# Performance work log

Measured on AMD Instinct MI355X. Metric: run time of the kernel, lower is better.

Reference implementation:

```python
import jax, jax.numpy as jnp
import numpy as np

Q_HEADS, KV_HEADS, DIMS = 16, 4, 1024
HEAD_DIM = DIMS // Q_HEADS          # 64
GROUPS = Q_HEADS // KV_HEADS        # 4
ROPE_BASE = 10000.0


def rope(x):
    # x: (..., s, d) -- standard interleaved rotary embedding, base 10000
    s, d = x.shape[-2], x.shape[-1]
    inv_freq = 1.0 / (ROPE_BASE ** (jnp.arange(0, d, 2, dtype=jnp.float32) / d))
    ang = jnp.arange(s, dtype=jnp.float32)[:, None] * inv_freq[None, :]  # (s, d/2)
    cos, sin = jnp.cos(ang), jnp.sin(ang)
    x1, x2 = x[..., 0::2], x[..., 1::2]
    out = jnp.stack([x1 * cos - x2 * sin, x1 * sin + x2 * cos], axis=-1)
    return out.reshape(x.shape).astype(x.dtype)


def setup_inputs() -> dict:
    key = jax.random.key(0)
    k1, k2, k3, k4, k5, k6 = jax.random.split(key, 6)
    B, S, E = 4, 2048, 1024
    q = jax.random.normal(k1, (B, S, E), dtype=jnp.float32)
    kv = jax.random.normal(k2, (B, S, E), dtype=jnp.float32)
    sc = 1.0 / np.sqrt(E)
    Wq = jax.random.normal(k3, (E, Q_HEADS, HEAD_DIM), dtype=jnp.float32) * sc
    Wk = jax.random.normal(k4, (E, KV_HEADS, HEAD_DIM), dtype=jnp.float32) * sc
    Wv = jax.random.normal(k5, (E, KV_HEADS, HEAD_DIM), dtype=jnp.float32) * sc
    Wo = jax.random.normal(k6, (HEAD_DIM, E), dtype=jnp.float32) / np.sqrt(HEAD_DIM)
    return {"q": q, "kv": kv, "Wq": Wq, "Wk": Wk, "Wv": Wv, "Wo": Wo}


def reference(q, kv, Wq, Wk, Wv, Wo):
    B, S, E = q.shape
    qh = jnp.einsum('bse,ehd->bshd', q, Wq)    # (B,S,Q_HEADS,hd)
    kh = jnp.einsum('bse,ehd->bshd', kv, Wk)   # (B,S,KV_HEADS,hd)
    vh = jnp.einsum('bse,ehd->bshd', kv, Wv)
    # rearrange '... s (h g) d -> ... g h s d' with g=GROUPS (h = KV_HEADS outer)
    qh = qh.reshape(B, S, KV_HEADS, GROUPS, HEAD_DIM).transpose(0, 3, 2, 1, 4)  # (B,g,h,S,d)
    kh = kh.transpose(0, 2, 1, 3)  # (B,h,S,d)
    vh = vh.transpose(0, 2, 1, 3)  # (B,h,S,d)
    qh = rope(qh)
    kh = rope(kh)
    # NOTE: sums over group axis g (faithful to original einsum)
    scores = jnp.einsum('bghsd,bhad->bhsa', qh, kh)
    attn = jax.nn.softmax(scores / (HEAD_DIM ** 0.5), axis=-1)
    out = jnp.einsum('bhsa,bhad->bhsd', attn, vh)  # (B,h,S,d)
    out = out.mean(axis=1)                          # mean over kv heads -> (B,S,d)
    return out @ Wo                                 # (B,S,E)
```

## Files before the change

### kernel.cpp

```cpp
#include <hip/hip_runtime.h>
#include <math.h>

#define SS 2048
#define EE 1024

using bf16x8 = __attribute__((ext_vector_type(8))) short;
using f32x4  = __attribute__((ext_vector_type(4))) float;

__device__ inline short f2bf(float x) {
    unsigned u = __builtin_bit_cast(unsigned, x);
    return (short)((u + 0x7fffu + ((u >> 16) & 1u)) >> 16);
}
__device__ inline short f2bf_r(float x) {
    return (short)((__builtin_bit_cast(unsigned, x) + 0x8000u) >> 16);
}
__device__ inline unsigned pk_bf16(float a, float b) {
    unsigned ua = __builtin_bit_cast(unsigned, a) + 0x8000u;
    unsigned ub = __builtin_bit_cast(unsigned, b) + 0x8000u;
    return __builtin_amdgcn_perm(ub, ua, 0x07060302u);
}
__device__ inline void gl16(const short* g, short* l) {
    __builtin_amdgcn_global_load_lds(
        (const __attribute__((address_space(1))) void*)g,
        (__attribute__((address_space(3))) void*)l, 16, 0, 0);
}

__global__ __launch_bounds__(256) void prep_weights(const float* __restrict__ q,
                                                    const float* __restrict__ kv,
                                                    const float* __restrict__ Wq,
                                                    const float* __restrict__ Wk,
                                                    const float* __restrict__ Wv,
                                                    const float* __restrict__ Wo,
                                                    short* __restrict__ Ab,
                                                    short* __restrict__ Wall,
                                                    short* __restrict__ Wo4,
                                                    float2* __restrict__ RT) {
    if (blockIdx.x < 8192) {
        int gt = blockIdx.x * 256 + threadIdx.x;
        size_t e0 = (size_t)gt * 8;
        const float* src = (e0 < 8388608) ? (q + e0) : (kv + (e0 - 8388608));
        float4 v0 = *(const float4*)src;
        float4 v1 = *(const float4*)(src + 4);
        int4 u;
        u.x = pk_bf16(v0.x, v0.y);
        u.y = pk_bf16(v0.z, v0.w);
        u.z = pk_bf16(v1.x, v1.y);
        u.w = pk_bf16(v1.z, v1.w);
        *(int4*)&Ab[e0] = u;
        return;
    }
    int idx = (blockIdx.x - 8192) * 256 + threadIdx.x;
    int c = idx >> 10, e = idx & 1023;
    int h = c >> 6, d = c & 63;
    const float* p = Wq + (size_t)e * 1024 + h * 256 + d;
    Wall[(size_t)c * 1024 + e] = f2bf(0.18033688011112042f * (p[0] + p[64] + p[128] + p[192]));
    Wall[(size_t)(256 + c) * 1024 + e] = f2bf(Wk[(size_t)e * 256 + c]);
    Wall[(size_t)(512 + c) * 1024 + e] = f2bf(Wv[(size_t)e * 256 + c]);
    Wo4[(size_t)e * 256 + c] = f2bf(0.25f * Wo[(size_t)d * 1024 + e]);
    if (idx < 65536) {
        int s = idx >> 5, ii = idx & 31;
        float freq = __expf(-(float)ii * (9.210340371976184f / 32.0f));
        float sn, cs;
        sincosf((float)s * freq, &sn, &cs);
        RT[idx] = (float2){cs, sn};
    }
}

__global__ __launch_bounds__(256) void proj_kernel(const short* __restrict__ Ab,
                                                   const short* __restrict__ Wall,
                                                   const float2* __restrict__ RT,
                                                   short* __restrict__ Qb,
                                                   short* __restrict__ Kb,
                                                   short* __restrict__ Vt) {
    __shared__ alignas(16) short SMEM[128 * 64 + 64 * 64];
    short (*As)[64] = (short (*)[64])SMEM;
    short (*Bs)[64] = (short (*)[64])(SMEM + 128 * 64);
    int tid = threadIdx.x;
    int wave = tid >> 6, lane = tid & 63, quad = lane >> 4, c16 = lane & 15;
    int wm = wave >> 1, wn = wave & 1;
    int m0 = blockIdx.x * 128, n0 = blockIdx.y * 64;
    const short* A = Ab + ((n0 < 256) ? 0 : (size_t)8388608);

    int lr = lane >> 3, lc = lane & 7;
    f32x4 acc[4][2];
    #pragma unroll
    for (int i = 0; i < 4; i++)
        #pragma unroll
        for (int j = 0; j < 2; j++) acc[i][j] = (f32x4){0.f, 0.f, 0.f, 0.f};

    for (int k0 = 0; k0 < 1024; k0 += 64) {
        __syncthreads();
        #pragma unroll
        for (int i = 0; i < 4; i++) {
            int seg = wave * 4 + i;
            int r = seg * 8 + lr;
            gl16(&A[(size_t)(m0 + r) * 1024 + k0 + lc * 8], &As[seg * 8][0]);
        }
        #pragma unroll
        for (int i = 0; i < 2; i++) {
            int seg = wave * 2 + i;
            int r = seg * 8 + lr;
            gl16(&Wall[(size_t)(n0 + r) * 1024 + k0 + lc * 8], &Bs[seg * 8][0]);
        }
        __syncthreads();
        #pragma unroll
        for (int ks = 0; ks < 64; ks += 32) {
            bf16x8 af[4], bfr[2];
            #pragma unroll
            for (int mt = 0; mt < 4; mt++)
                af[mt] = *(const bf16x8*)&As[wm * 64 + mt * 16 + c16][ks + quad * 8];
            #pragma unroll
            for (int nt = 0; nt < 2; nt++)
                bfr[nt] = *(const bf16x8*)&Bs[wn * 32 + nt * 16 + c16][ks + quad * 8];
            #pragma unroll
            for (int mt = 0; mt < 4; mt++)
                #pragma unroll
                for (int nt = 0; nt < 2; nt++)
                    acc[mt][nt] = __builtin_amdgcn_mfma_f32_16x16x32_bf16(
                        af[mt], bfr[nt], acc[mt][nt], 0, 0, 0);
        }
    }
    __syncthreads();
    if (n0 < 512) {
        #pragma unroll
        for (int mt = 0; mt < 4; mt++) {
            #pragma unroll
            for (int nt = 0; nt < 2; nt++) {
                int cl = wn * 32 + nt * 16 + c16;
                int ii = cl >> 1;
                float sgn = (lane & 1) ? 1.0f : -1.0f;
                f32x4 v = acc[mt][nt];
                #pragma unroll
                for (int r = 0; r < 4; r++) {
                    int rl = wm * 64 + mt * 16 + quad * 4 + r;
                    float2 cs = RT[((m0 + rl) & (SS - 1)) * 32 + ii];
                    float other = __shfl_xor(v[r], 1);
                    As[rl][cl] = f2bf_r(v[r] * cs.x + sgn * cs.y * other);
                }
            }
        }
        __syncthreads();
        short* dstb = (n0 < 256) ? Qb : Kb;
        int nc0 = n0 & 255;
        #pragma unroll
        for (int i = 0; i < 4; i++) {
            int id = i * 256 + tid, r = id >> 3, ch = id & 7;
            *(int4*)&dstb[(size_t)(m0 + r) * 256 + nc0 + ch * 8] =
                *(const int4*)&As[r][ch * 8];
        }
    } else {
        short (*Lt)[136] = (short(*)[136])SMEM;
        #pragma unroll
        for (int mt = 0; mt < 4; mt++) {
            #pragma unroll
            for (int nt = 0; nt < 2; nt++) {
                int cl = wn * 32 + nt * 16 + c16;
                int sl = wm * 64 + mt * 16 + quad * 4;
                f32x4 v = acc[mt][nt];
                uint2 u;
                u.x = pk_bf16(v[0], v[1]);
                u.y = pk_bf16(v[2], v[3]);
                *(uint2*)&Lt[cl][sl] = u;
            }
        }
        __syncthreads();
        int b = m0 >> 11, s0 = m0 & (SS - 1), c0 = n0 - 512;
        #pragma unroll
        for (int i = 0; i < 4; i++) {
            int id = i * 256 + tid, c = id >> 4, ch = id & 15;
            *(int4*)&Vt[((size_t)(b * 256 + c0 + c)) * SS + s0 + ch * 8] =
                *(const int4*)&Lt[c][ch * 8];
        }
    }
}

__global__ __launch_bounds__(512, 4) void attn_kernel(const short* __restrict__ Qb,
                                                      const short* __restrict__ Kb,
                                                      const short* __restrict__ Vt,
                                                      short* __restrict__ Ob) {
    __shared__ alignas(16) short SM[24576];
    short (*Qs)[64] = (short (*)[64])SM;
    short (*Ps2)[64] = (short (*)[64])(SM + 4096);
    short (*Ks)[64][64] = (short (*)[64][64])(SM + 8192);
    short (*Vs)[64][64] = (short (*)[64][64])(SM + 16384);
    int tid = threadIdx.x;
    int wave = tid >> 6, lane = tid & 63, quad = lane >> 4, c16 = lane & 15;
    int rq = wave & 3, kh = wave >> 2;
    int qt = blockIdx.x, bh = blockIdx.y;
    int q0 = qt * 64;
    size_t qkbase = (size_t)(bh >> 2) * SS * 256 + (bh & 3) * 64;
    size_t vtbase = (size_t)(bh * 64) * SS;

    {
        int r = tid >> 3, ch = tid & 7;
        *(int4*)&Qs[r][ch * 8] = *(const int4*)&Qb[qkbase + (size_t)(q0 + r) * 256 + ch * 8];
    }
    __syncthreads();
    bf16x8 aq0 = *(const bf16x8*)&Qs[rq * 16 + c16][quad * 8];
    bf16x8 aq1 = *(const bf16x8*)&Qs[rq * 16 + c16][32 + quad * 8];
    short (*Ps)[64] = (kh == 0) ? (short (*)[64])Qs[rq * 16] : (short (*)[64])Ps2[rq * 16];

    int swz = (c16 & 7) << 3;

    float lsum[4] = {0.f, 0.f, 0.f, 0.f};
    f32x4 o[4];
    #pragma unroll
    for (int dt = 0; dt < 4; dt++) o[dt] = (f32x4){0.f, 0.f, 0.f, 0.f};

    int sr = tid >> 3, sch = tid & 7;
    int wsz = (sch * 8) ^ ((sr & 7) << 3);
    int4 kr0 = *(const int4*)&Kb[qkbase + (size_t)sr * 256 + sch * 8];
    int4 kr1 = *(const int4*)&Kb[qkbase + (size_t)(1024 + sr) * 256 + sch * 8];
    int4 vr0 = *(const int4*)&Vt[vtbase + (size_t)sr * SS + sch * 8];
    int4 vr1 = *(const int4*)&Vt[vtbase + (size_t)sr * SS + 1024 + sch * 8];

    for (int kt = 0; kt < 16; kt++) {
        __syncthreads();
        *(int4*)&Ks[0][sr][wsz] = kr0;
        *(int4*)&Ks[1][sr][wsz] = kr1;
        *(int4*)&Vs[0][sr][wsz] = vr0;
        *(int4*)&Vs[1][sr][wsz] = vr1;
        if (kt < 15) {
            int a1 = (kt + 1) * 64;
            kr0 = *(const int4*)&Kb[qkbase + (size_t)(a1 + sr) * 256 + sch * 8];
            kr1 = *(const int4*)&Kb[qkbase + (size_t)(1024 + a1 + sr) * 256 + sch * 8];
            vr0 = *(const int4*)&Vt[vtbase + (size_t)sr * SS + a1 + sch * 8];
            vr1 = *(const int4*)&Vt[vtbase + (size_t)sr * SS + 1024 + a1 + sch * 8];
        }
        __syncthreads();
        f32x4 sv[4];
        #pragma unroll
        for (int nt = 0; nt < 4; nt++) sv[nt] = (f32x4){0.f, 0.f, 0.f, 0.f};
        __builtin_amdgcn_s_setprio(1);
        #pragma unroll
        for (int nt = 0; nt < 4; nt++) {
            bf16x8 bk0 = *(const bf16x8*)&Ks[kh][nt * 16 + c16][(quad * 8) ^ swz];
            bf16x8 bk1 = *(const bf16x8*)&Ks[kh][nt * 16 + c16][(32 + quad * 8) ^ swz];
            sv[nt] = __builtin_amdgcn_mfma_f32_16x16x32_bf16(aq0, bk0, sv[nt], 0, 0, 0);
            sv[nt] = __builtin_amdgcn_mfma_f32_16x16x32_bf16(aq1, bk1, sv[nt], 0, 0, 0);
        }
        __builtin_amdgcn_s_setprio(0);
        #pragma unroll
        for (int nt = 0; nt < 4; nt++)
            #pragma unroll
            for (int r = 0; r < 4; r++) sv[nt][r] = __builtin_exp2f(sv[nt][r]);
        #pragma unroll
        for (int r = 0; r < 4; r++)
            lsum[r] += (sv[0][r] + sv[1][r]) + (sv[2][r] + sv[3][r]);
        #pragma unroll
        for (int nt = 0; nt < 4; nt++)
            #pragma unroll
            for (int r = 0; r < 4; r++) {
                int lrow = quad * 4 + r;
                Ps[lrow][(nt * 16 + c16) ^ ((lrow & 7) << 3)] = f2bf_r(sv[nt][r]);
            }
        #pragma unroll
        for (int ks = 0; ks < 64; ks += 32) {
            bf16x8 ap = *(const bf16x8*)&Ps[c16][(ks + quad * 8) ^ swz];
            __builtin_amdgcn_s_setprio(1);
            #pragma unroll
            for (int dt = 0; dt < 4; dt++) {
                bf16x8 bv = *(const bf16x8*)&Vs[kh][dt * 16 + c16][(ks + quad * 8) ^ swz];
                o[dt] = __builtin_amdgcn_mfma_f32_16x16x32_bf16(ap, bv, o[dt], 0, 0, 0);
            }
            __builtin_amdgcn_s_setprio(0);
        }
    }
    #pragma unroll
    for (int off = 1; off < 16; off <<= 1)
        #pragma unroll
        for (int r = 0; r < 4; r++) lsum[r] += __shfl_xor(lsum[r], off);

    __syncthreads();
    float (*Ox)[68] = (float (*)[68])SM;
    float* Lx = (float*)(SM + 9216);
    short (*Ot)[72] = (short (*)[72])(SM + 12288);
    int base = rq * 16 + quad * 4;
    if (wave >= 4) {
        #pragma unroll
        for (int dt = 0; dt < 4; dt++)
            #pragma unroll
            for (int r = 0; r < 4; r++)
                Ox[base + r][dt * 16 + c16] = o[dt][r];
        if (c16 == 0)
            #pragma unroll
            for (int r = 0; r < 4; r++) Lx[base + r] = lsum[r];
    }
    __syncthreads();
    if (wave < 4) {
        #pragma unroll
        for (int r = 0; r < 4; r++) {
            float rl = __builtin_amdgcn_rcpf(lsum[r] + Lx[base + r]);
            #pragma unroll
            for (int dt = 0; dt < 4; dt++)
                Ot[base + r][dt * 16 + c16] =
                    f2bf_r((o[dt][r] + Ox[base + r][dt * 16 + c16]) * rl);
        }
    }
    __syncthreads();
    {
        int r = tid >> 3, ch = tid & 7;
        int b = bh >> 2, h = bh & 3;
        *(int4*)&Ob[((size_t)(b * SS + q0 + r)) * 256 + h * 64 + ch * 8] =
            *(const int4*)&Ot[r][ch * 8];
    }
}

__global__ __launch_bounds__(256) void outproj_kernel(const short* __restrict__ Ob,
                                                      const short* __restrict__ Wo4,
                                                      float* __restrict__ out) {
    __shared__ alignas(16) short As[128][72];
    __shared__ alignas(16) short Bs[64][72];
    int tid = threadIdx.x;
    int wave = tid >> 6, lane = tid & 63, quad = lane >> 4, c16 = lane & 15;
    int m0 = blockIdx.x * 128, n0 = blockIdx.y * 64;

    f32x4 acc[2][4];
    #pragma unroll
    for (int i = 0; i < 2; i++)
        #pragma unroll
        for (int j = 0; j < 4; j++) acc[i][j] = (f32x4){0.f, 0.f, 0.f, 0.f};

    for (int k0 = 0; k0 < 256; k0 += 64) {
        #pragma unroll
        for (int i = 0; i < 4; i++) {
            int id = i * 256 + tid, r = id >> 3, ch = id & 7;
            *(int4*)&As[r][ch * 8] =
                *(const int4*)&Ob[(size_t)(m0 + r) * 256 + k0 + ch * 8];
        }
        #pragma unroll
        for (int i = 0; i < 2; i++) {
            int id = i * 256 + tid, r = id >> 3, ch = id & 7;
            *(int4*)&Bs[r][ch * 8] =
                *(const int4*)&Wo4[(size_t)(n0 + r) * 256 + k0 + ch * 8];
        }
        __syncthreads();
        #pragma unroll
        for (int ks = 0; ks < 64; ks += 32) {
            bf16x8 af[2], bfr[4];
            #pragma unroll
            for (int mt = 0; mt < 2; mt++)
                af[mt] = *(const bf16x8*)&As[wave * 32 + mt * 16 + c16][ks + quad * 8];
            #pragma unroll
            for (int nt = 0; nt < 4; nt++)
                bfr[nt] = *(const bf16x8*)&Bs[nt * 16 + c16][ks + quad * 8];
            #pragma unroll
            for (int mt = 0; mt < 2; mt++)
                #pragma unroll
                for (int nt = 0; nt < 4; nt++)
                    acc[mt][nt] = __builtin_amdgcn_mfma_f32_16x16x32_bf16(
                        af[mt], bfr[nt], acc[mt][nt], 0, 0, 0);
        }
        __syncthreads();
    }
    #pragma unroll
    for (int mt = 0; mt < 2; mt++)
        #pragma unroll
        for (int nt = 0; nt < 4; nt++) {
            int col = n0 + nt * 16 + c16;
            int rowb = m0 + wave * 32 + mt * 16 + quad * 4;
            #pragma unroll
            for (int r = 0; r < 4; r++)
                out[(size_t)(rowb + r) * 1024 + col] = acc[mt][nt][r];
        }
}

extern "C" void kernel_launch(void* const* d_in, const int* in_sizes, int n_in,
                              void* d_out, int out_size, void* d_ws, size_t ws_size,
                              hipStream_t stream) {
    const float* q  = (const float*)d_in[0];
    const float* kv = (const float*)d_in[1];
    const float* Wq = (const float*)d_in[2];
    const float* Wk = (const float*)d_in[3];
    const float* Wv = (const float*)d_in[4];
    const float* Wo = (const float*)d_in[5];
    float* out = (float*)d_out;

    short* Qb    = (short*)d_ws;
    short* Kb    = Qb + 2097152;
    short* Vt    = Kb + 2097152;
    short* Wall  = Vt + 2097152;
    short* Wo4   = Wall + 786432;
    float2* RT   = (float2*)(Wo4 + 262144);
    short* Ob    = (short*)(RT + 65536);
    short* Ab    = Ob + 2097152;

    prep_weights<<<9216, 256, 0, stream>>>(q, kv, Wq, Wk, Wv, Wo, Ab, Wall, Wo4, RT);

    proj_kernel<<<dim3(64, 12), 256, 0, stream>>>(Ab, Wall, RT, Qb, Kb, Vt);

    attn_kernel<<<dim3(32, 16), 512, 0, stream>>>(Qb, Kb, Vt, Ob);

    outproj_kernel<<<dim3(64, 16), 256, 0, stream>>>(Ob, Wo4, out);
}
```

Baseline: 193.4 us.

## Double-buffer K/V tiles in attention and remap blocks for XCD locality

```diff
diff --git a/kernel.cpp b/kernel.cpp
--- a/kernel.cpp
+++ b/kernel.cpp
@@ -78,7 +78,9 @@
     int tid = threadIdx.x;
     int wave = tid >> 6, lane = tid & 63, quad = lane >> 4, c16 = lane & 15;
     int wm = wave >> 1, wn = wave & 1;
-    int m0 = blockIdx.x * 128, n0 = blockIdx.y * 64;
+    int lin = blockIdx.y * 64 + blockIdx.x;
+    int X = lin & 7, rr = lin >> 3;
+    int m0 = (X * 8 + rr / 12) * 128, n0 = (rr % 12) * 64;
     const short* A = Ab + ((n0 < 256) ? 0 : (size_t)8388608);
 
     int lr = lane >> 3, lc = lane & 7;
@@ -178,27 +180,24 @@
                                                       const short* __restrict__ Kb,
                                                       const short* __restrict__ Vt,
                                                       short* __restrict__ Ob) {
-    __shared__ alignas(16) short SM[24576];
-    short (*Qs)[64] = (short (*)[64])SM;
-    short (*Ps2)[64] = (short (*)[64])(SM + 4096);
-    short (*Ks)[64][64] = (short (*)[64][64])(SM + 8192);
-    short (*Vs)[64][64] = (short (*)[64][64])(SM + 16384);
+    __shared__ alignas(16) short SM[40960];
+    short (*Ks)[2][64][64] = (short (*)[2][64][64])(SM + 8192);
+    short (*Vs)[2][64][64] = (short (*)[2][64][64])(SM + 24576);
     int tid = threadIdx.x;
     int wave = tid >> 6, lane = tid & 63, quad = lane >> 4, c16 = lane & 15;
     int rq = wave & 3, kh = wave >> 2;
-    int qt = blockIdx.x, bh = blockIdx.y;
+    int lin = blockIdx.y * 32 + blockIdx.x;
+    int X = lin & 7, rr = lin >> 3;
+    int bh = X * 2 + (rr >> 5), qt = rr & 31;
     int q0 = qt * 64;
     size_t qkbase = (size_t)(bh >> 2) * SS * 256 + (bh & 3) * 64;
     size_t vtbase = (size_t)(bh * 64) * SS;
 
-    {
-        int r = tid >> 3, ch = tid & 7;
-        *(int4*)&Qs[r][ch * 8] = *(const int4*)&Qb[qkbase + (size_t)(q0 + r) * 256 + ch * 8];
-    }
-    __syncthreads();
-    bf16x8 aq0 = *(const bf16x8*)&Qs[rq * 16 + c16][quad * 8];
-    bf16x8 aq1 = *(const bf16x8*)&Qs[rq * 16 + c16][32 + quad * 8];
-    short (*Ps)[64] = (kh == 0) ? (short (*)[64])Qs[rq * 16] : (short (*)[64])Ps2[rq * 16];
+    const short* qrow = Qb + qkbase + (size_t)(q0 + rq * 16 + c16) * 256 + quad * 8;
+    bf16x8 aq0 = *(const bf16x8*)qrow;
+    bf16x8 aq1 = *(const bf16x8*)(qrow + 32);
+
+    short (*Ps)[64] = (short (*)[64])(SM + wave * 1024);
 
     int swz = (c16 & 7) << 3;
 
@@ -209,33 +208,47 @@
 
     int sr = tid >> 3, sch = tid & 7;
     int wsz = (sch * 8) ^ ((sr & 7) << 3);
-    int4 kr0 = *(const int4*)&Kb[qkbase + (size_t)sr * 256 + sch * 8];
-    int4 kr1 = *(const int4*)&Kb[qkbase + (size_t)(1024 + sr) * 256 + sch * 8];
-    int4 vr0 = *(const int4*)&Vt[vtbase + (size_t)sr * SS + sch * 8];
-    int4 vr1 = *(const int4*)&Vt[vtbase + (size_t)sr * SS + 1024 + sch * 8];
-
+    const short* kbase = Kb + qkbase;
+    const short* vbase = Vt + vtbase + (size_t)sr * SS;
+
+    int4 kr0 = *(const int4*)&kbase[(size_t)sr * 256 + sch * 8];
+    int4 kr1 = *(const int4*)&kbase[(size_t)(1024 + sr) * 256 + sch * 8];
+    int4 vr0 = *(const int4*)&vbase[sch * 8];
+    int4 vr1 = *(const int4*)&vbase[1024 + sch * 8];
+    *(int4*)&Ks[0][0][sr][wsz] = kr0;
+    *(int4*)&Ks[0][1][sr][wsz] = kr1;
+    *(int4*)&Vs[0][0][sr][wsz] = vr0;
+    *(int4*)&Vs[0][1][sr][wsz] = vr1;
+    kr0 = *(const int4*)&kbase[(size_t)(64 + sr) * 256 + sch * 8];
+    kr1 = *(const int4*)&kbase[(size_t)(1024 + 64 + sr) * 256 + sch * 8];
+    vr0 = *(const int4*)&vbase[64 + sch * 8];
+    vr1 = *(const int4*)&vbase[1024 + 64 + sch * 8];
+    __syncthreads();
+
+    #pragma unroll 1
     for (int kt = 0; kt < 16; kt++) {
-        __syncthreads();
-        *(int4*)&Ks[0][sr][wsz] = kr0;
-        *(int4*)&Ks[1][sr][wsz] = kr1;
-        *(int4*)&Vs[0][sr][wsz] = vr0;
-        *(int4*)&Vs[1][sr][wsz] = vr1;
+        int p = kt & 1;
         if (kt < 15) {
-            int a1 = (kt + 1) * 64;
-            kr0 = *(const int4*)&Kb[qkbase + (size_t)(a1 + sr) * 256 + sch * 8];
-            kr1 = *(const int4*)&Kb[qkbase + (size_t)(1024 + a1 + sr) * 256 + sch * 8];
-            vr0 = *(const int4*)&Vt[vtbase + (size_t)sr * SS + a1 + sch * 8];
-            vr1 = *(const int4*)&Vt[vtbase + (size_t)sr * SS + 1024 + a1 + sch * 8];
-        }
-        __syncthreads();
+            *(int4*)&Ks[p ^ 1][0][sr][wsz] = kr0;
+            *(int4*)&Ks[p ^ 1][1][sr][wsz] = kr1;
+            *(int4*)&Vs[p ^ 1][0][sr][wsz] = vr0;
+            *(int4*)&Vs[p ^ 1][1][sr][wsz] = vr1;
+        }
+        if (kt < 14) {
+            int a1 = (kt + 2) * 64;
+            kr0 = *(const int4*)&kbase[(size_t)(a1 + sr) * 256 + sch * 8];
+            kr1 = *(const int4*)&kbase[(size_t)(1024 + a1 + sr) * 256 + sch * 8];
+            vr0 = *(const int4*)&vbase[a1 + sch * 8];
+            vr1 = *(const int4*)&vbase[1024 + a1 + sch * 8];
+        }
         f32x4 sv[4];
         #pragma unroll
         for (int nt = 0; nt < 4; nt++) sv[nt] = (f32x4){0.f, 0.f, 0.f, 0.f};
         __builtin_amdgcn_s_setprio(1);
         #pragma unroll
         for (int nt = 0; nt < 4; nt++) {
-            bf16x8 bk0 = *(const bf16x8*)&Ks[kh][nt * 16 + c16][(quad * 8) ^ swz];
-            bf16x8 bk1 = *(const bf16x8*)&Ks[kh][nt * 16 + c16][(32 + quad * 8) ^ swz];
+            bf16x8 bk0 = *(const bf16x8*)&Ks[p][kh][nt * 16 + c16][(quad * 8) ^ swz];
+            bf16x8 bk1 = *(const bf16x8*)&Ks[p][kh][nt * 16 + c16][(32 + quad * 8) ^ swz];
             sv[nt] = __builtin_amdgcn_mfma_f32_16x16x32_bf16(aq0, bk0, sv[nt], 0, 0, 0);
             sv[nt] = __builtin_amdgcn_mfma_f32_16x16x32_bf16(aq1, bk1, sv[nt], 0, 0, 0);
         }
@@ -260,18 +273,18 @@
             __builtin_amdgcn_s_setprio(1);
             #pragma unroll
             for (int dt = 0; dt < 4; dt++) {
-                bf16x8 bv = *(const bf16x8*)&Vs[kh][dt * 16 + c16][(ks + quad * 8) ^ swz];
+                bf16x8 bv = *(const bf16x8*)&Vs[p][kh][dt * 16 + c16][(ks + quad * 8) ^ swz];
                 o[dt] = __builtin_amdgcn_mfma_f32_16x16x32_bf16(ap, bv, o[dt], 0, 0, 0);
             }
             __builtin_amdgcn_s_setprio(0);
         }
+        __syncthreads();
     }
     #pragma unroll
     for (int off = 1; off < 16; off <<= 1)
         #pragma unroll
         for (int r = 0; r < 4; r++) lsum[r] += __shfl_xor(lsum[r], off);
 
-    __syncthreads();
     float (*Ox)[68] = (float (*)[68])SM;
     float* Lx = (float*)(SM + 9216);
     short (*Ot)[72] = (short (*)[72])(SM + 12288);
@@ -313,7 +326,9 @@
     __shared__ alignas(16) short Bs[64][72];
     int tid = threadIdx.x;
     int wave = tid >> 6, lane = tid & 63, quad = lane >> 4, c16 = lane & 15;
-    int m0 = blockIdx.x * 128, n0 = blockIdx.y * 64;
+    int lin = blockIdx.y * 64 + blockIdx.x;
+    int X = lin & 7, rr = lin >> 3;
+    int m0 = (X * 8 + (rr >> 4)) * 128, n0 = (rr & 15) * 64;
 
     f32x4 acc[2][4];
     #pragma unroll
```

Result: no change. 192.5 us (-0.4%).
